# Performance work log

Hardware: AMD Instinct MI355X
Metric: run time of the kernel (lower is better)

The kernel has to match this reference:

```python
import jax, jax.numpy as jnp
import numpy as np

SURROGATE_ALPHA = 2.0  # ATan surrogate sharpness (spikingjelly-style default)

@jax.custom_vjp
def spike_fn(x):
    return jnp.where(x > 0, 1.0, 0.0)

def _spike_fwd(x):
    return spike_fn(x), x

def _spike_bwd(x, g):
    # ATan surrogate gradient: alpha/2 / (1 + (pi/2 * alpha * x)^2)
    sg = SURROGATE_ALPHA / 2.0 / (1.0 + (jnp.pi / 2.0 * SURROGATE_ALPHA * x) ** 2)
    return (g * sg,)

spike_fn.defvjp(_spike_fwd, _spike_bwd)

def setup_inputs() -> dict:
    key = jax.random.key(0)
    B, N, T, D = 4, 1024, 128, 128  # [batch, nodes, time, feat]
    x = jax.random.normal(key, (B, N, T, D), dtype=jnp.float32)
    decay = jnp.zeros((D,), jnp.float32)  # nn.initializers.constant(0.0)
    v_th = jnp.zeros((D,), jnp.float32)   # nn.initializers.constant(0.0)
    return {"x": x, "decay": decay, "v_th": v_th}

def reference(x, decay, v_th):
    # time axis is dim 2 in the original module
    x_seq = jnp.moveaxis(x, 2, 0)  # [T, B, N, D]
    d = jax.nn.sigmoid(decay)          # per-feature learnable decay in (0,1)
    th = jax.nn.sigmoid(v_th) + 0.1    # per-feature learnable threshold > 0.1

    def scan_fn(v, x_t):
        v = v * d + x_t                        # leaky integrate
        s = spike_fn(v - th)                   # fire
        v = v * (1.0 - jax.lax.stop_gradient(s))  # hard reset (detached)
        return v, s

    v_init = jnp.zeros_like(x_seq[0])
    _, spikes = jax.lax.scan(scan_fn, v_init, x_seq)
    return jnp.moveaxis(spikes, 0, 2)  # back to [B, N, T, D]
```

## Files before the change

### kernel.cpp

```cpp
#include <hip/hip_runtime.h>
#include <math.h>


#define T_STEPS 128
#define D_FEAT  128
#define CT      16
#define CTD     (CT * D_FEAT)
#define NCHUNK  (T_STEPS / CT)

typedef float f32x4 __attribute__((ext_vector_type(4)));

__global__ __launch_bounds__(256)
void plif_fwd_kernel(const f32x4* __restrict__ x4,
                     const float* __restrict__ decay,
                     const float* __restrict__ vth,
                     f32x4* __restrict__ out4)
{
    __shared__ float xs[2 * CTD];

    const int tid  = threadIdx.x;
    const int lrow = tid >> 7;
    const int d    = tid & (D_FEAT - 1);
    const int r0   = blockIdx.x * 2;

    const float dec = 1.0f / (1.0f + expf(-decay[d]));
    const float th  = 1.0f / (1.0f + expf(-vth[d])) + 0.1f;

    const size_t rowq = (size_t)T_STEPS * D_FEAT / 4;

    float v = 0.0f;

    for (int c = 0; c < NCHUNK; ++c) {
        const size_t cq = (size_t)c * (CTD / 4);

#pragma unroll
        for (int p = 0; p < 4; ++p) {
            const int rr   = p >> 1;
            const int slot = (p & 1) * 256 + tid;
            const f32x4 tmp = __builtin_nontemporal_load(
                x4 + (size_t)(r0 + rr) * rowq + cq + (size_t)slot);
            *(f32x4*)&xs[rr * CTD + slot * 4] = tmp;
        }
        __syncthreads();

#pragma unroll
        for (int i = 0; i < CT; ++i) {
            const int idx = lrow * CTD + i * D_FEAT + d;
            const float xv = xs[idx];
            v = __fadd_rn(__fmul_rn(v, dec), xv);
            const bool f = (v > th);
            xs[idx] = f ? 1.0f : 0.0f;
            v = f ? 0.0f : v;
        }
        __syncthreads();

#pragma unroll
        for (int p = 0; p < 4; ++p) {
            const int rr   = p >> 1;
            const int slot = (p & 1) * 256 + tid;
            const f32x4 sv = *(const f32x4*)&xs[rr * CTD + slot * 4];
            __builtin_nontemporal_store(sv,
                out4 + (size_t)(r0 + rr) * rowq + cq + (size_t)slot);
        }
    }
}

extern "C" void kernel_launch(void* const* d_in, const int* in_sizes, int n_in,
                              void* d_out, int out_size, void* d_ws, size_t ws_size,
                              hipStream_t stream)
{
    const float* x     = (const float*)d_in[0];
    const float* decay = (const float*)d_in[1];
    const float* vth   = (const float*)d_in[2];
    float*       out   = (float*)d_out;

    const int total  = in_sizes[0];
    const int rows   = total / (T_STEPS * D_FEAT);
    const int blocks = rows / 2;
    const int block  = 256;

    plif_fwd_kernel<<<blocks, block, 0, stream>>>(
        (const f32x4*)x, decay, vth, (f32x4*)out);
}
```

Before: 97.20 us.

## Assign one wavefront per row and drop block barriers in PLIF scan

Each 64-lane wavefront now owns a whole (b,n) row, with every lane handling two features. The staging buffer in LDS is private to that wavefront, so both __syncthreads barriers per chunk go away, and the chunk size shrinks from 16 to 8 timesteps. Each block covers four rows instead of two. In exchange there is half as much thread-level parallelism per row and the sequential scan gets longer per thread, and correctness depends on wavefront-synchronous LDS access with no explicit barrier.

```diff
diff --git a/kernel.cpp b/kernel.cpp
--- a/kernel.cpp
+++ b/kernel.cpp
@@ -4,10 +4,11 @@
 
 #define T_STEPS 128
 #define D_FEAT  128
-#define CT      16
+#define CT      8
 #define CTD     (CT * D_FEAT)
 #define NCHUNK  (T_STEPS / CT)
 
+typedef float f32x2 __attribute__((ext_vector_type(2)));
 typedef float f32x4 __attribute__((ext_vector_type(4)));
 
 __global__ __launch_bounds__(256)
@@ -16,51 +17,58 @@
                      const float* __restrict__ vth,
                      f32x4* __restrict__ out4)
 {
-    __shared__ float xs[2 * CTD];
+    __shared__ float xs[4][CTD];
 
-    const int tid  = threadIdx.x;
-    const int lrow = tid >> 7;
-    const int d    = tid & (D_FEAT - 1);
-    const int r0   = blockIdx.x * 2;
+    const int tid = threadIdx.x;
+    const int w   = tid >> 6;
+    const int l   = tid & 63;
+    const int row = blockIdx.x * 4 + w;
+    const int d0  = l * 2;
 
-    const float dec = 1.0f / (1.0f + expf(-decay[d]));
-    const float th  = 1.0f / (1.0f + expf(-vth[d])) + 0.1f;
+    const float decA = 1.0f / (1.0f + expf(-decay[d0 + 0]));
+    const float decB = 1.0f / (1.0f + expf(-decay[d0 + 1]));
+    const float thA  = 1.0f / (1.0f + expf(-vth[d0 + 0])) + 0.1f;
+    const float thB  = 1.0f / (1.0f + expf(-vth[d0 + 1])) + 0.1f;
 
     const size_t rowq = (size_t)T_STEPS * D_FEAT / 4;
+    const f32x4* __restrict__ xr  = x4  + (size_t)row * rowq;
+    f32x4* __restrict__       orw = out4 + (size_t)row * rowq;
 
-    float v = 0.0f;
+    float* __restrict__ mylds = xs[w];
+
+    float vA = 0.0f, vB = 0.0f;
 
     for (int c = 0; c < NCHUNK; ++c) {
         const size_t cq = (size_t)c * (CTD / 4);
 
 #pragma unroll
         for (int p = 0; p < 4; ++p) {
-            const int rr   = p >> 1;
-            const int slot = (p & 1) * 256 + tid;
-            const f32x4 tmp = __builtin_nontemporal_load(
-                x4 + (size_t)(r0 + rr) * rowq + cq + (size_t)slot);
-            *(f32x4*)&xs[rr * CTD + slot * 4] = tmp;
+            const f32x4 tmp = __builtin_nontemporal_load(xr + cq + p * 64 + l);
+            *(f32x4*)&mylds[(p * 64 + l) * 4] = tmp;
         }
-        __syncthreads();
 
 #pragma unroll
         for (int i = 0; i < CT; ++i) {
-            const int idx = lrow * CTD + i * D_FEAT + d;
-            const float xv = xs[idx];
-            v = __fadd_rn(__fmul_rn(v, dec), xv);
-            const bool f = (v > th);
-            xs[idx] = f ? 1.0f : 0.0f;
-            v = f ? 0.0f : v;
+            const f32x2 xv = *(const f32x2*)&mylds[i * D_FEAT + d0];
+
+            vA = __fadd_rn(__fmul_rn(vA, decA), xv.x);
+            const bool fA = (vA > thA);
+            const float sA = fA ? 1.0f : 0.0f;
+            vA = fA ? 0.0f : vA;
+
+            vB = __fadd_rn(__fmul_rn(vB, decB), xv.y);
+            const bool fB = (vB > thB);
+            const float sB = fB ? 1.0f : 0.0f;
+            vB = fB ? 0.0f : vB;
+
+            f32x2 sv; sv.x = sA; sv.y = sB;
+            *(f32x2*)&mylds[i * D_FEAT + d0] = sv;
         }
-        __syncthreads();
 
 #pragma unroll
         for (int p = 0; p < 4; ++p) {
-            const int rr   = p >> 1;
-            const int slot = (p & 1) * 256 + tid;
-            const f32x4 sv = *(const f32x4*)&xs[rr * CTD + slot * 4];
-            __builtin_nontemporal_store(sv,
-                out4 + (size_t)(r0 + rr) * rowq + cq + (size_t)slot);
+            const f32x4 sv = *(const f32x4*)&mylds[(p * 64 + l) * 4];
+            __builtin_nontemporal_store(sv, orw + cq + p * 64 + l);
         }
     }
 }
@@ -76,7 +84,7 @@
 
     const int total  = in_sizes[0];
     const int rows   = total / (T_STEPS * D_FEAT);
-    const int blocks = rows / 2;
+    const int blocks = rows / 4;
     const int block  = 256;
 
     plif_fwd_kernel<<<blocks, block, 0, stream>>>(
```

After: 113.0 us. 16.2% more time.
